# Kernel optimization log

Measured on AMD Instinct MI355X. Metric: run time of the kernel, lower is better.

## Reference

```python
import jax, jax.numpy as jnp
import numpy as np

N, E = 50000, 800000
IN, MAP, H, O = 256, 64, 4, 64
LEAKY_SLOPE = 0.2


def setup_inputs() -> dict:
    key = jax.random.key(0)
    ks = jax.random.split(key, 12)
    x = jax.random.normal(ks[0], (N, IN), dtype=jnp.float32)
    src = jax.random.randint(ks[1], (E,), 0, N, dtype=jnp.int32)
    dst = jax.random.randint(ks[2], (E,), 0, N, dtype=jnp.int32)
    s = 1.0 / np.sqrt(IN)
    W_gat = jax.random.normal(ks[3], (IN, H * O), dtype=jnp.float32) * s
    attn_l = jax.random.normal(ks[4], (H, O), dtype=jnp.float32) * 0.1
    attn_r = jax.random.normal(ks[5], (H, O), dtype=jnp.float32) * 0.1
    gate_m_W = jax.random.normal(ks[6], (IN, MAP), dtype=jnp.float32) * s
    gate_m_b = jnp.zeros((MAP,), dtype=jnp.float32)
    gate_fn_W = jax.random.normal(ks[7], (2 * IN + MAP, H), dtype=jnp.float32) * (1.0 / np.sqrt(2 * IN + MAP))
    gate_fn_b = jnp.zeros((H,), dtype=jnp.float32)
    merge_W = jax.random.normal(ks[8], (IN + O, O), dtype=jnp.float32) * (1.0 / np.sqrt(IN + O))
    merge_b = jnp.zeros((O,), dtype=jnp.float32)
    return {"x": x, "src": src, "dst": dst, "W_gat": W_gat, "attn_l": attn_l,
            "attn_r": attn_r, "gate_m_W": gate_m_W, "gate_m_b": gate_m_b,
            "gate_fn_W": gate_fn_W, "gate_fn_b": gate_fn_b,
            "merge_W": merge_W, "merge_b": merge_b}


def _forward(x, src, dst, W_gat, attn_l, attn_r, gate_m_W, gate_m_b,
             gate_fn_W, gate_fn_b, merge_W, merge_b):
    n = x.shape[0]
    # --- gate branch: gspmm mean of x, gspmm max of linear_z over in-neighbors ---
    deg = jax.ops.segment_sum(jnp.ones_like(dst, dtype=x.dtype), dst, num_segments=n)
    mean_z = jax.ops.segment_sum(x[src], dst, num_segments=n) / jnp.maximum(deg, 1.0)[:, None]
    z = x @ gate_m_W + gate_m_b  # [N, MAP]
    max_z = jax.ops.segment_max(z[src], dst, num_segments=n)
    max_z = jnp.where(deg[:, None] > 0, max_z, 0.0)  # empty neighborhoods -> 0
    nft = jnp.concatenate([x, max_z, mean_z], axis=1)  # [N, 2*IN+MAP]
    gate = jax.nn.sigmoid(nft @ gate_fn_W + gate_fn_b)  # [N, H]
    # --- GATConv ---
    feat = (x @ W_gat).reshape(n, H, O)  # [N, H, O]
    el = jnp.einsum('nho,ho->nh', feat, attn_l)
    er = jnp.einsum('nho,ho->nh', feat, attn_r)
    e = jax.nn.leaky_relu(el[src] + er[dst], negative_slope=LEAKY_SLOPE)  # [E, H]
    m = jax.ops.segment_max(e, dst, num_segments=n)  # [N, H]
    m = jnp.where(jnp.isfinite(m), m, 0.0)
    ex = jnp.exp(e - m[dst])  # [E, H]
    s = jax.ops.segment_sum(ex, dst, num_segments=n)  # [N, H]
    alpha = ex / jnp.maximum(s[dst], 1e-16)  # [E, H]
    attn_out = jax.ops.segment_sum(feat[src] * alpha[:, :, None], dst, num_segments=n)  # [N, H, O]
    # --- gated merge ---
    gated = (gate[:, :, None] * attn_out).mean(axis=1)  # [N, O]
    merge = jnp.concatenate([x, gated], axis=1) @ merge_W + merge_b  # [N, O]
    return merge


def reference(x, src, dst, W_gat, attn_l, attn_r, gate_m_W, gate_m_b,
              gate_fn_W, gate_fn_b, merge_W, merge_b):
    return _forward(x, src, dst, W_gat, attn_l, attn_r, gate_m_W, gate_m_b,
                    gate_fn_W, gate_fn_b, merge_W, merge_b)
```

## Files before the change

### kernel.cpp

```cpp
#include <hip/hip_runtime.h>
#include <math.h>

#define NN 50000
#define NE 800000
#define LEAKY 0.2f
#define NT 26
#define CAP 96
#define NBT (8 * NT * 64)
#define NB1 391
#define S1E 2048
#define NBUCK 196
#define EBMAX 5120
#define PREP_BLKS (55 + NB1)
#define GEMM_USED 1564
#define FUSE_BLKS 1764

typedef short bf16x8 __attribute__((ext_vector_type(8)));
typedef float f32x4 __attribute__((ext_vector_type(4)));
typedef float f32x2 __attribute__((ext_vector_type(2)));

__device__ __forceinline__ unsigned short f2bf(float f) {
  unsigned u = __float_as_uint(f);
  u += 0x7fffu + ((u >> 16) & 1u);
  return (unsigned short)(u >> 16);
}
__device__ __forceinline__ float leaky(float v) { return v > 0.0f ? v : LEAKY * v; }
__device__ __forceinline__ float rlf(float v, int l) {
  return __uint_as_float(__builtin_amdgcn_readlane(__float_as_uint(v), l));
}
__device__ __forceinline__ int rli(int v, int l) {
  return __builtin_amdgcn_readlane(v, l);
}

__device__ __forceinline__ bf16x8 cvt8(float4 fa, float4 fb) {
  unsigned r0, r1, r2, r3;
  asm("v_cvt_pk_bf16_f32 %0, %1, %2" : "=v"(r0) : "v"(fa.x), "v"(fa.y));
  asm("v_cvt_pk_bf16_f32 %0, %1, %2" : "=v"(r1) : "v"(fa.z), "v"(fa.w));
  asm("v_cvt_pk_bf16_f32 %0, %1, %2" : "=v"(r2) : "v"(fb.x), "v"(fb.y));
  asm("v_cvt_pk_bf16_f32 %0, %1, %2" : "=v"(r3) : "v"(fb.z), "v"(fb.w));
  union { uint4 u; bf16x8 v; } c;
  c.u = make_uint4(r0, r1, r2, r3);
  return c.v;
}

#if defined(__has_builtin)
#if __has_builtin(__builtin_amdgcn_cvt_pk_f32_fp8) && \
    __has_builtin(__builtin_amdgcn_cvt_pk_fp8_f32) && \
    __has_builtin(__builtin_amdgcn_cvt_f32_fp8)
#define FP8_HW 1
#endif
#endif

#ifdef FP8_HW
__device__ __forceinline__ unsigned char f2fp8(float v) {
  return (unsigned char)(__builtin_amdgcn_cvt_pk_fp8_f32(v, v, 0u, false) & 0xFF);
}
__device__ __forceinline__ f32x2 fp8x2_lo(unsigned int v) {
  return __builtin_amdgcn_cvt_pk_f32_fp8(v, false);
}
__device__ __forceinline__ f32x2 fp8x2_hi(unsigned int v) {
  return __builtin_amdgcn_cvt_pk_f32_fp8(v, true);
}
__device__ __forceinline__ float fp8one(unsigned int v) {
  return __builtin_amdgcn_cvt_f32_fp8(v, 0);
}
#else
__device__ __forceinline__ unsigned char f2fp8(float f) {
  unsigned u = __float_as_uint(f);
  unsigned s = (u >> 31) << 7;
  unsigned a = u & 0x7FFFFFFFu;
  if (a >= 0x43E00000u) return (unsigned char)(s | 0x7E);
  if (a < 0x3C800000u) {
    float m = __uint_as_float(a) * 512.0f;
    int q = (int)(m + 0.5f); if (q > 7) q = 7;
    return (unsigned char)(s | q);
  }
  a += 0x7FFFFu + ((a >> 20) & 1);
  unsigned e = ((a >> 23) & 0xFF) - 120;
  if (e > 15) return (unsigned char)(s | 0x7E);
  return (unsigned char)(s | (e << 3) | ((a >> 20) & 7));
}
__device__ __forceinline__ float fp8dec1(unsigned b) {
  unsigned s = (b & 0x80u) << 24;
  unsigned em = b & 0x7Fu;
  unsigned e4 = em >> 3, m3 = em & 7;
  float v = e4 ? __uint_as_float(((e4 + 120) << 23) | (m3 << 20))
               : (float)m3 * 0.001953125f;
  return __uint_as_float(__float_as_uint(v) ^ s);
}
__device__ __forceinline__ f32x2 fp8x2_lo(unsigned int v) {
  f32x2 r; r[0] = fp8dec1(v & 0xFF); r[1] = fp8dec1((v >> 8) & 0xFF); return r;
}
__device__ __forceinline__ f32x2 fp8x2_hi(unsigned int v) {
  f32x2 r; r[0] = fp8dec1((v >> 16) & 0xFF); r[1] = fp8dec1((v >> 24) & 0xFF); return r;
}
__device__ __forceinline__ float fp8one(unsigned int v) { return fp8dec1(v & 0xFF); }
#endif

__device__ __forceinline__ float dot64v(const float* __restrict__ w,
                                        const float* __restrict__ a) {
  float4 p0 = {0.f, 0.f, 0.f, 0.f};
#pragma unroll
  for (int o = 0; o < 64; o += 4) {
    float4 wv = *(const float4*)(w + o);
    float4 av = *(const float4*)(a + o);
    p0.x += wv.x * av.x; p0.y += wv.y * av.y;
    p0.z += wv.z * av.z; p0.w += wv.w * av.w;
  }
  return (p0.x + p0.y) + (p0.z + p0.w);
}
__device__ __forceinline__ float panel_w(int col, int k,
    const float* W_gat, const float* gate_m_W, const float* merge_W,
    const float* gate_fn_W, const float* attn_l, const float* attn_r) {
  if (col < 256)      return W_gat[k * 256 + (col & 3) * 64 + (col >> 2)];
  else if (col < 320) return gate_m_W[k * 64 + (col - 256)];
  else if (col < 384) return merge_W[k * 64 + (col - 320)];
  else if (col < 388) return gate_fn_W[k * 4 + (col - 384)];
  else if (col < 392) return gate_fn_W[(320 + k) * 4 + (col - 388)];
  else if (col < 396) {
    int h = col - 392;
    return dot64v(W_gat + k * 256 + h * 64, attn_l + h * 64);
  } else if (col < 400) {
    int h = col - 396;
    return dot64v(W_gat + k * 256 + h * 64, attn_r + h * 64);
  }
  return 0.0f;
}

__global__ __launch_bounds__(256) void k_prep_s1(
    const float* __restrict__ W_gat, const float* __restrict__ gate_m_W,
    const float* __restrict__ merge_W, const float* __restrict__ gate_fn_W,
    const float* __restrict__ attn_l, const float* __restrict__ attn_r,
    unsigned short* __restrict__ Btf, unsigned short* __restrict__ mWf,
    unsigned char* __restrict__ zq, float* __restrict__ epay,
    unsigned char* __restrict__ featq,
    const int* __restrict__ src, const int* __restrict__ dst,
    unsigned int* __restrict__ staged, unsigned short* __restrict__ bofs) {
  int b = blockIdx.x, tid = threadIdx.x;
  if (b < 54) {
    int idx = b * 256 + tid;
    if (idx < NBT) {
      int kq = idx / (NT * 64);
      int rem = idx - kq * (NT * 64);
      int t = rem >> 6, lane = rem & 63;
      int col = t * 16 + (lane & 15);
      int k = kq * 32 + (lane >> 4) * 8;
      unsigned short* o = Btf + (size_t)idx * 8;
#pragma unroll
      for (int i = 0; i < 8; ++i)
        o[i] = f2bf(panel_w(col, k + i, W_gat, gate_m_W, merge_W, gate_fn_W,
                            attn_l, attn_r));
    } else {
      int idx2 = idx - NBT;
      int kq = idx2 >> 8;
      int rem = idx2 & 255;
      int t = rem >> 6, lane = rem & 63;
      int col = t * 16 + (lane & 15);
      int k = kq * 32 + ((lane >> 4) & 3) * 8;
      unsigned short* o = mWf + (size_t)idx2 * 8;
#pragma unroll
      for (int i = 0; i < 8; ++i)
        o[i] = f2bf(merge_W[(size_t)(256 + k + i) * 64 + col]);
    }
  } else if (b == 54) {
    if (tid < 64) zq[(size_t)NN * 64 + tid] = 0xFE;
    if (tid < 8) epay[(size_t)NN * 8 + tid] = 0.0f;
    featq[(size_t)NN * 256 + tid] = 0;
  } else {
    __shared__ int hist[NBUCK], cntb[NBUCK], pfx[NBUCK], sc[256];
    __shared__ unsigned staged_l[S1E];
    int s1b = b - 55;
    int e0 = s1b * S1E;
    int cntE = NE - e0; if (cntE > S1E) cntE = S1E;
    for (int i = tid; i < NBUCK; i += 256) { hist[i] = 0; cntb[i] = 0; }
    __syncthreads();
    int myn[8], mys[8];
#pragma unroll
    for (int j = 0; j < 8; ++j) {
      int li = j * 256 + tid;
      bool valid = li < cntE;
      myn[j] = valid ? dst[e0 + li] : -1;
      mys[j] = valid ? src[e0 + li] : 0;
      if (valid) atomicAdd(&hist[myn[j] >> 8], 1);
    }
    __syncthreads();
    int v = (tid < NBUCK) ? hist[tid] : 0;
    sc[tid] = v; __syncthreads();
#pragma unroll
    for (int off = 1; off < 256; off <<= 1) {
      int t = (tid >= off) ? sc[tid - off] : 0;
      __syncthreads();
      sc[tid] += t;
      __syncthreads();
    }
    if (tid < NBUCK) pfx[tid] = sc[tid] - v;
    __syncthreads();
#pragma unroll
    for (int j = 0; j < 8; ++j) {
      if (myn[j] >= 0) {
        int bk = myn[j] >> 8;
        int p = pfx[bk] + atomicAdd(&cntb[bk], 1);
        staged_l[p] = ((unsigned)mys[j] << 8) | (unsigned)(myn[j] & 255);
      }
    }
    __syncthreads();
    for (int i = tid; i < cntE; i += 256) staged[(size_t)e0 + i] = staged_l[i];
    for (int i = tid; i < NBUCK + 1; i += 256)
      bofs[(size_t)s1b * (NBUCK + 1) + i] =
          (unsigned short)((i < NBUCK) ? pfx[i] : cntE);
  }
}

#define EBW 22528
union FusedLDS {
  unsigned short ldsB[2][13][64][8];
  struct {
    unsigned eb[EBMAX];
    int cnt2[256];
    int sc[256];
  } s2;
};

__global__ __launch_bounds__(256, 3) void k_gemm_s2(
    const float* __restrict__ x, const unsigned short* __restrict__ Btf,
    const float* __restrict__ gate_m_b,
    unsigned char* __restrict__ featq, unsigned char* __restrict__ zq,
    float* __restrict__ xm, float* __restrict__ gx, float* __restrict__ epay,
    float* __restrict__ erv,
    const unsigned int* __restrict__ staged, const unsigned short* __restrict__ bofs,
    int* __restrict__ deg, unsigned short* __restrict__ csr_src) {
  __shared__ FusedLDS L;
  int tid = threadIdx.x;
  int b = blockIdx.x;
  if (b % 9 == 8) {
    int bk = b / 9;
    int nb0 = bk << 8;
    int mycnt[2], myofs[2];
#pragma unroll
    for (int k = 0; k < 2; ++k) {
      int bi = tid + k * 256;
      if (bi < NB1) {
        int o  = bofs[(size_t)bi * (NBUCK + 1) + bk];
        int n1 = bofs[(size_t)bi * (NBUCK + 1) + bk + 1];
        myofs[k] = o; mycnt[k] = n1 - o;
      } else { myofs[k] = 0; mycnt[k] = 0; }
    }
    int lsum = mycnt[0] + mycnt[1];
    L.s2.sc[tid] = lsum; __syncthreads();
#pragma unroll
    for (int off = 1; off < 256; off <<= 1) {
      int t = (tid >= off) ? L.s2.sc[tid - off] : 0;
      __syncthreads();
      L.s2.sc[tid] += t;
      __syncthreads();
    }
    int base = L.s2.sc[tid] - lsum;
    int Eb = L.s2.sc[255];
    if (Eb > EBMAX) Eb = EBMAX;
    int pos = base;
#pragma unroll
    for (int k = 0; k < 2; ++k) {
      int bi = tid + k * 256;
      for (int c = 0; c < mycnt[k]; ++c) {
        if (pos < EBMAX)
          L.s2.eb[pos] = staged[(size_t)bi * S1E + myofs[k] + c];
        ++pos;
      }
    }
    __syncthreads();
    L.s2.cnt2[tid] = 0;
    __syncthreads();
    for (int i = tid; i < Eb; i += 256) {
      unsigned v = L.s2.eb[i];
      int nl = v & 255;
      int p = atomicAdd(&L.s2.cnt2[nl], 1);
      if (p < CAP)
        csr_src[(size_t)(nb0 + nl) * CAP + p] = (unsigned short)(v >> 8);
    }
    __syncthreads();
    int n = nb0 + tid;
    if (n < NN) {
      int d = L.s2.cnt2[tid];
      deg[n] = d < CAP ? d : CAP;
    }
    return;
  }
  int bq = b - b / 9;
  if (bq >= GEMM_USED) return;
  int rb = bq >> 1, ch = bq & 1;
  int lane = tid & 63, wave = tid >> 6;
  int m = lane & 15, kg = lane >> 4;
  int rowB = rb * 64;
  int t0 = ch * 13;
  int arow = rowB + wave * 16 + m;
  if (arow >= NN) arow = NN - 1;
  const float* aP = x + (size_t)arow * 256 + kg * 8;

  f32x4 acc[13];
  f32x4 zero = {0.f, 0.f, 0.f, 0.f};
#pragma unroll
  for (int t = 0; t < 13; ++t) acc[t] = zero;

  for (int t = wave; t < 13; t += 4)
    __builtin_amdgcn_global_load_lds(
        (const __attribute__((address_space(1))) unsigned int*)
            (Btf + ((size_t)(t0 + t)) * 512 + lane * 8),
        (__attribute__((address_space(3))) unsigned int*)(&L.ldsB[0][t][0][0]),
        16, 0, 0);
  float4 fa = *(const float4*)aP;
  float4 fb = *(const float4*)(aP + 4);
  __syncthreads();

#pragma unroll 1
  for (int kq = 0; kq < 8; ++kq) {
    int cur = kq & 1;
    int kqn = kq < 7 ? kq + 1 : 7;
    float4 fa_n = *(const float4*)(aP + kqn * 32);
    float4 fb_n = *(const float4*)(aP + kqn * 32 + 4);
    if (kq < 7) {
      for (int t = wave; t < 13; t += 4)
        __builtin_amdgcn_global_load_lds(
            (const __attribute__((address_space(1))) unsigned int*)
                (Btf + ((size_t)(kq + 1) * NT + t0 + t) * 512 + lane * 8),
            (__attribute__((address_space(3))) unsigned int*)
                (&L.ldsB[cur ^ 1][t][0][0]),
            16, 0, 0);
    }
    bf16x8 a = cvt8(fa, fb);
#pragma unroll
    for (int t = 0; t < 13; ++t) {
      bf16x8 bfr = *(const bf16x8*)&L.ldsB[cur][t][lane][0];
      acc[t] = __builtin_amdgcn_mfma_f32_16x16x32_bf16(a, bfr, acc[t], 0, 0, 0);
    }
    fa = fa_n; fb = fb_n;
    __syncthreads();
  }

  if (ch == 0) {
#pragma unroll
    for (int r = 0; r < 4; ++r) {
      int row = rowB + wave * 16 + kg * 4 + r;
      if (row >= NN) continue;
#pragma unroll
      for (int t = 0; t < 13; ++t)
        featq[(size_t)row * 256 + t * 16 + m] = f2fp8(acc[t][r]);
    }
  } else {
#pragma unroll
    for (int r = 0; r < 4; ++r) {
      int row = rowB + wave * 16 + kg * 4 + r;
      if (row >= NN) continue;
#pragma unroll
      for (int t = 0; t < 3; ++t)
        featq[(size_t)row * 256 + 208 + t * 16 + m] = f2fp8(acc[t][r]);
#pragma unroll
      for (int t = 3; t < 7; ++t) {
        int cc = (t - 3) * 16 + m;
        zq[(size_t)row * 64 + cc] = f2fp8(acc[t][r] + gate_m_b[cc]);
      }
#pragma unroll
      for (int t = 7; t < 11; ++t)
        xm[(size_t)row * 64 + (t - 7) * 16 + m] = acc[t][r];
      float v = acc[11][r];
      if (m < 4)       gx[(size_t)row * 4 + m] = v;
      else if (m < 8)  epay[(size_t)row * 8 + (m - 4) * 2 + 1] = v;
      else if (m < 12) epay[(size_t)row * 8 + (m - 8) * 2] = v;
      else             erv[(size_t)row * 4 + (m - 12)] = v;
    }
  }
}

__global__ __launch_bounds__(256) void k_node(
    const unsigned char* __restrict__ zq, const unsigned char* __restrict__ featq,
    const float* __restrict__ epay, const float* __restrict__ er,
    const float* __restrict__ gx,
    const int* __restrict__ deg, const unsigned short* __restrict__ csr_src,
    const float* __restrict__ gate_fn_W, const float* __restrict__ gate_fn_b,
    const unsigned short* __restrict__ mWf, const float* __restrict__ xm,
    const float* __restrict__ merge_b, float* __restrict__ out) {
  __shared__ float WzT[4][64];
  __shared__ float pbuf[4][16][4];
  __shared__ unsigned short gLDS[16][72];
  int tid = threadIdx.x;
  {
    int c = tid >> 2, h = tid & 3;
    WzT[h][c] = gate_fn_W[(256 + c) * 4 + h];
  }
  __syncthreads();

  int lane = tid & 63, wave = tid >> 6;
  int hh = lane >> 4, le = lane & 15;
  int rowbase = blockIdx.x * 16;
  int nodeBase = rowbase + wave * 4;
#pragma unroll 1
  for (int i = 0; i < 4; ++i) {
    int node = nodeBase + i;
    int dg = deg[node]; if (dg > CAP) dg = CAP;
    float gated = 0.0f;
    if (dg > 0) {
      int rs = node * CAP, re = rs + dg;
      float er_h = er[(size_t)node * 4 + hh];
      f32x2 A01 = {0.f, 0.f}, A23 = {0.f, 0.f};
      float psum = 0, usum = 0;
      float mz = -INFINITY;
      int jj = rs + le;
      int s_l = (jj < re) ? (int)csr_src[jj] : NN;
#pragma unroll 1
      for (int j0 = rs; j0 < re; j0 += 16) {
        int jn = j0 + 16 + le;
        int s_nx = (jn < re) ? (int)csr_src[jn] : NN;
        bool valid = (j0 + le) < re;
        float2 eu = *(const float2*)(epay + ((size_t)(unsigned)s_l << 3) + hh * 2);
        float p = valid ? __expf(leaky(eu.x + er_h)) : 0.0f;
        psum += p;
        usum += eu.y;
        pbuf[wave][le][hh] = p;
        unsigned int fvr[16];
        unsigned int zvr[16];
#pragma unroll
        for (int e2 = 0; e2 < 16; ++e2) {
          int s = rli(s_l, e2);
          fvr[e2] = *(const unsigned int*)(featq + ((size_t)(unsigned)s << 8) + lane * 4);
        }
#pragma unroll
        for (int e2 = 0; e2 < 16; ++e2) {
          int s = rli(s_l, e2);
          zvr[e2] = zq[((size_t)(unsigned)s << 6) + lane];
        }
#pragma unroll
        for (int e2 = 0; e2 < 16; ++e2) {
          float4 pv = *(const float4*)pbuf[wave][e2];
          f32x2 p01 = {pv.x, pv.y};
          f32x2 p23 = {pv.z, pv.w};
          A01 += p01 * fp8x2_lo(fvr[e2]);
          A23 += p23 * fp8x2_hi(fvr[e2]);
          mz = fmaxf(mz, fp8one(zvr[e2]));
        }
        s_l = s_nx;
      }
#pragma unroll
      for (int off = 1; off < 16; off <<= 1) {
        psum += __shfl_xor(psum, off, 64);
        usum += __shfl_xor(usum, off, 64);
      }
      float s0 = rlf(psum, 0),  s1 = rlf(psum, 16);
      float s2 = rlf(psum, 32), s3 = rlf(psum, 48);
      float su0 = rlf(usum, 0),  su1 = rlf(usum, 16);
      float su2 = rlf(usum, 32), su3 = rlf(usum, 48);

      float g[4];
#pragma unroll
      for (int h = 0; h < 4; ++h) {
        float t = mz * WzT[h][lane];
#pragma unroll
        for (int off = 32; off; off >>= 1) t += __shfl_xor(t, off, 64);
        g[h] = t;
      }
      float inv_deg = 1.0f / (float)dg;
      float4 gx4 = *(const float4*)(gx + (size_t)node * 4);
      float g0 = 1.0f / (1.0f + __expf(-(g[0] + gx4.x + su0 * inv_deg + gate_fn_b[0])));
      float g1 = 1.0f / (1.0f + __expf(-(g[1] + gx4.y + su1 * inv_deg + gate_fn_b[1])));
      float g2 = 1.0f / (1.0f + __expf(-(g[2] + gx4.z + su2 * inv_deg + gate_fn_b[2])));
      float g3 = 1.0f / (1.0f + __expf(-(g[3] + gx4.w + su3 * inv_deg + gate_fn_b[3])));
      gated = 0.25f * (g0 * A01[0] / s0 + g1 * A01[1] / s1 +
                       g2 * A23[0] / s2 + g3 * A23[1] / s3);
    }
    gLDS[wave * 4 + i][lane] = f2bf(gated);
  }
  __syncthreads();

  int m = lane & 15, kg = lane >> 4;
  f32x4 acc = {0.f, 0.f, 0.f, 0.f};
#pragma unroll
  for (int kq = 0; kq < 2; ++kq) {
    bf16x8 a = *(const bf16x8*)(&gLDS[m][kq * 32 + kg * 8]);
    bf16x8 b = *(const bf16x8*)(mWf + (((size_t)kq * 4 + wave) * 64 + lane) * 8);
    acc = __builtin_amdgcn_mfma_f32_16x16x32_bf16(a, b, acc, 0, 0, 0);
  }
  int c = wave * 16 + m;
  float mb = merge_b[c];
#pragma unroll
  for (int r = 0; r < 4; ++r) {
    int row = rowbase + kg * 4 + r;
    out[(size_t)row * 64 + c] = acc[r] + xm[(size_t)row * 64 + c] + mb;
  }
}

extern "C" void kernel_launch(void* const* d_in, const int* in_sizes, int n_in,
                              void* d_out, int out_size, void* d_ws, size_t ws_size,
                              hipStream_t stream) {
  const float* x         = (const float*)d_in[0];
  const int*   src       = (const int*)d_in[1];
  const int*   dst       = (const int*)d_in[2];
  const float* W_gat     = (const float*)d_in[3];
  const float* attn_l    = (const float*)d_in[4];
  const float* attn_r    = (const float*)d_in[5];
  const float* gate_m_W  = (const float*)d_in[6];
  const float* gate_m_b  = (const float*)d_in[7];
  const float* gate_fn_W = (const float*)d_in[8];
  const float* gate_fn_b = (const float*)d_in[9];
  const float* merge_W   = (const float*)d_in[10];
  const float* merge_b   = (const float*)d_in[11];
  float* out = (float*)d_out;

  char* ws = (char*)d_ws;
  size_t off = 0;
  auto alloc = [&](size_t bytes) -> void* {
    off = (off + 255) & ~(size_t)255;
    void* p = ws + off;
    off += bytes;
    return p;
  };
  int* deg       = (int*)alloc((size_t)NN * 4);
  unsigned short* csr_src = (unsigned short*)alloc((size_t)NN * CAP * 2);
  unsigned int* staged    = (unsigned int*)alloc((size_t)NE * 4);
  unsigned short* bofs    = (unsigned short*)alloc((size_t)NB1 * (NBUCK + 1) * 2);
  float* epay = (float*)alloc((size_t)(NN + 1) * 8 * 4);
  float* er   = (float*)alloc((size_t)NN * 4 * 4);
  float* gx   = (float*)alloc((size_t)NN * 4 * 4);
  float* xm   = (float*)alloc((size_t)NN * 64 * 4);
  unsigned char* zq    = (unsigned char*)alloc((size_t)(NN + 1) * 64);
  unsigned char* featq = (unsigned char*)alloc((size_t)(NN + 1) * 256);
  unsigned short* Btf    = (unsigned short*)alloc((size_t)NBT * 8 * 2);
  unsigned short* mWf    = (unsigned short*)alloc((size_t)512 * 8 * 2);

  k_prep_s1<<<PREP_BLKS, 256, 0, stream>>>(W_gat, gate_m_W, merge_W, gate_fn_W,
                                           attn_l, attn_r, Btf, mWf, zq, epay,
                                           featq, src, dst, staged, bofs);
  k_gemm_s2<<<FUSE_BLKS, 256, 0, stream>>>(x, Btf, gate_m_b,
                                           featq, zq, xm, gx, epay, er,
                                           staged, bofs, deg, csr_src);
  k_node<<<NN / 16, 256, 0, stream>>>(zq, featq, epay, er, gx, deg, csr_src,
                                      gate_fn_W, gate_fn_b, mWf, xm, merge_b, out);
}
```

Before: 234.2 us.

## Split GEMM into four column groups with register-resident B fragments instead of LDS

The fused GEMM kernel now splits each 64-row block's 26 output tiles into four column groups of 7 tiles (with overlap), rather than two halves of 13. B fragments are loaded straight from global memory into registers with double buffering, dropping the LDS staging and per-iteration barriers. The CSR-building blocks are moved to the first 196 block indices instead of being interleaved every ninth block. This gives more, lighter blocks with fewer accumulators to improve occupancy and remove sync stalls. The cost is redundant A-row loads across four blocks, some duplicated tile computation, and more global B traffic.

Result: no change. 238.5 us (+1.8%).

```diff
diff --git a/kernel.cpp b/kernel.cpp
--- a/kernel.cpp
+++ b/kernel.cpp
@@ -12,8 +12,8 @@
 #define NBUCK 196
 #define EBMAX 5120
 #define PREP_BLKS (55 + NB1)
-#define GEMM_USED 1564
-#define FUSE_BLKS 1764
+#define S2_BLKS 196
+#define FUSE_BLKS 3332
 
 typedef short bf16x8 __attribute__((ext_vector_type(8)));
 typedef float f32x4 __attribute__((ext_vector_type(4)));
@@ -211,16 +211,6 @@
   }
 }
 
-#define EBW 22528
-union FusedLDS {
-  unsigned short ldsB[2][13][64][8];
-  struct {
-    unsigned eb[EBMAX];
-    int cnt2[256];
-    int sc[256];
-  } s2;
-};
-
 __global__ __launch_bounds__(256, 3) void k_gemm_s2(
     const float* __restrict__ x, const unsigned short* __restrict__ Btf,
     const float* __restrict__ gate_m_b,
@@ -229,11 +219,15 @@
     float* __restrict__ erv,
     const unsigned int* __restrict__ staged, const unsigned short* __restrict__ bofs,
     int* __restrict__ deg, unsigned short* __restrict__ csr_src) {
-  __shared__ FusedLDS L;
+  __shared__ struct {
+    unsigned eb[EBMAX];
+    int cnt2[256];
+    int sc[256];
+  } L;
   int tid = threadIdx.x;
   int b = blockIdx.x;
-  if (b % 9 == 8) {
-    int bk = b / 9;
+  if (b < S2_BLKS) {
+    int bk = b;
     int nb0 = bk << 8;
     int mycnt[2], myofs[2];
 #pragma unroll
@@ -246,16 +240,16 @@
       } else { myofs[k] = 0; mycnt[k] = 0; }
     }
     int lsum = mycnt[0] + mycnt[1];
-    L.s2.sc[tid] = lsum; __syncthreads();
+    L.sc[tid] = lsum; __syncthreads();
 #pragma unroll
     for (int off = 1; off < 256; off <<= 1) {
-      int t = (tid >= off) ? L.s2.sc[tid - off] : 0;
+      int t = (tid >= off) ? L.sc[tid - off] : 0;
       __syncthreads();
-      L.s2.sc[tid] += t;
+      L.sc[tid] += t;
       __syncthreads();
     }
-    int base = L.s2.sc[tid] - lsum;
-    int Eb = L.s2.sc[255];
+    int base = L.sc[tid] - lsum;
+    int Eb = L.sc[255];
     if (Eb > EBMAX) Eb = EBMAX;
     int pos = base;
 #pragma unroll
@@ -263,109 +257,96 @@
       int bi = tid + k * 256;
       for (int c = 0; c < mycnt[k]; ++c) {
         if (pos < EBMAX)
-          L.s2.eb[pos] = staged[(size_t)bi * S1E + myofs[k] + c];
+          L.eb[pos] = staged[(size_t)bi * S1E + myofs[k] + c];
         ++pos;
       }
     }
     __syncthreads();
-    L.s2.cnt2[tid] = 0;
+    L.cnt2[tid] = 0;
     __syncthreads();
     for (int i = tid; i < Eb; i += 256) {
-      unsigned v = L.s2.eb[i];
+      unsigned v = L.eb[i];
       int nl = v & 255;
-      int p = atomicAdd(&L.s2.cnt2[nl], 1);
+      int p = atomicAdd(&L.cnt2[nl], 1);
       if (p < CAP)
         csr_src[(size_t)(nb0 + nl) * CAP + p] = (unsigned short)(v >> 8);
     }
     __syncthreads();
     int n = nb0 + tid;
     if (n < NN) {
-      int d = L.s2.cnt2[tid];
+      int d = L.cnt2[tid];
       deg[n] = d < CAP ? d : CAP;
     }
     return;
   }
-  int bq = b - b / 9;
-  if (bq >= GEMM_USED) return;
-  int rb = bq >> 1, ch = bq & 1;
+  int bq = b - S2_BLKS;
+  int rb = (bq >> 5) * 8 + (bq & 7);
+  if (rb >= 782) return;
+  int q = (bq >> 3) & 3;
+  int tstart = (q == 0) ? 0 : (q == 1) ? 7 : (q == 2) ? 13 : 19;
   int lane = tid & 63, wave = tid >> 6;
   int m = lane & 15, kg = lane >> 4;
   int rowB = rb * 64;
-  int t0 = ch * 13;
   int arow = rowB + wave * 16 + m;
   if (arow >= NN) arow = NN - 1;
   const float* aP = x + (size_t)arow * 256 + kg * 8;
-
-  f32x4 acc[13];
+  const unsigned short* bB = Btf + ((size_t)(tstart * 64 + lane)) * 8;
+
+  f32x4 acc[7];
   f32x4 zero = {0.f, 0.f, 0.f, 0.f};
 #pragma unroll
-  for (int t = 0; t < 13; ++t) acc[t] = zero;
-
-  for (int t = wave; t < 13; t += 4)
-    __builtin_amdgcn_global_load_lds(
-        (const __attribute__((address_space(1))) unsigned int*)
-            (Btf + ((size_t)(t0 + t)) * 512 + lane * 8),
-        (__attribute__((address_space(3))) unsigned int*)(&L.ldsB[0][t][0][0]),
-        16, 0, 0);
+  for (int t = 0; t < 7; ++t) acc[t] = zero;
+
+  bf16x8 bC[7], bN[7];
   float4 fa = *(const float4*)aP;
   float4 fb = *(const float4*)(aP + 4);
-  __syncthreads();
-
+#pragma unroll
+  for (int t = 0; t < 7; ++t)
+    bC[t] = *(const bf16x8*)(bB + (size_t)t * 512);
 #pragma unroll 1
-  for (int kq = 0; kq < 8; ++kq) {
-    int cur = kq & 1;
-    int kqn = kq < 7 ? kq + 1 : 7;
-    float4 fa_n = *(const float4*)(aP + kqn * 32);
-    float4 fb_n = *(const float4*)(aP + kqn * 32 + 4);
-    if (kq < 7) {
-      for (int t = wave; t < 13; t += 4)
-        __builtin_amdgcn_global_load_lds(
-            (const __attribute__((address_space(1))) unsigned int*)
-                (Btf + ((size_t)(kq + 1) * NT + t0 + t) * 512 + lane * 8),
-            (__attribute__((address_space(3))) unsigned int*)
-                (&L.ldsB[cur ^ 1][t][0][0]),
-            16, 0, 0);
-    }
-    bf16x8 a = cvt8(fa, fb);
-#pragma unroll
-    for (int t = 0; t < 13; ++t) {
-      bf16x8 bfr = *(const bf16x8*)&L.ldsB[cur][t][lane][0];
-      acc[t] = __builtin_amdgcn_mfma_f32_16x16x32_bf16(a, bfr, acc[t], 0, 0, 0);
-    }
-    fa = fa_n; fb = fb_n;
-    __syncthreads();
-  }
-
-  if (ch == 0) {
-#pragma unroll
-    for (int r = 0; r < 4; ++r) {
-      int row = rowB + wave * 16 + kg * 4 + r;
-      if (row >= NN) continue;
-#pragma unroll
-      for (int t = 0; t < 13; ++t)
-        featq[(size_t)row * 256 + t * 16 + m] = f2fp8(acc[t][r]);
-    }
-  } else {
-#pragma unroll
-    for (int r = 0; r < 4; ++r) {
-      int row = rowB + wave * 16 + kg * 4 + r;
-      if (row >= NN) continue;
-#pragma unroll
-      for (int t = 0; t < 3; ++t)
-        featq[(size_t)row * 256 + 208 + t * 16 + m] = f2fp8(acc[t][r]);
-#pragma unroll
-      for (int t = 3; t < 7; ++t) {
-        int cc = (t - 3) * 16 + m;
-        zq[(size_t)row * 64 + cc] = f2fp8(acc[t][r] + gate_m_b[cc]);
+  for (int kq = 0; kq < 8; kq += 2) {
+    float4 fa1 = *(const float4*)(aP + (kq + 1) * 32);
+    float4 fb1 = *(const float4*)(aP + (kq + 1) * 32 + 4);
+#pragma unroll
+    for (int t = 0; t < 7; ++t)
+      bN[t] = *(const bf16x8*)(bB + ((size_t)(kq + 1) * NT + t) * 512);
+    bf16x8 a0 = cvt8(fa, fb);
+#pragma unroll
+    for (int t = 0; t < 7; ++t)
+      acc[t] = __builtin_amdgcn_mfma_f32_16x16x32_bf16(a0, bC[t], acc[t], 0, 0, 0);
+    int kq2 = kq + 2 < 8 ? kq + 2 : 7;
+    fa = *(const float4*)(aP + kq2 * 32);
+    fb = *(const float4*)(aP + kq2 * 32 + 4);
+#pragma unroll
+    for (int t = 0; t < 7; ++t)
+      bC[t] = *(const bf16x8*)(bB + ((size_t)kq2 * NT + t) * 512);
+    bf16x8 a1 = cvt8(fa1, fb1);
+#pragma unroll
+    for (int t = 0; t < 7; ++t)
+      acc[t] = __builtin_amdgcn_mfma_f32_16x16x32_bf16(a1, bN[t], acc[t], 0, 0, 0);
+  }
+
+#pragma unroll
+  for (int r = 0; r < 4; ++r) {
+    int row = rowB + wave * 16 + kg * 4 + r;
+    if (row >= NN) continue;
+#pragma unroll
+    for (int t = 0; t < 7; ++t) {
+      int tg = tstart + t;
+      float v = acc[t][r];
+      if (tg < 16) {
+        featq[(size_t)row * 256 + tg * 16 + m] = f2fp8(v);
+      } else if (tg < 20) {
+        int cc = (tg - 16) * 16 + m;
+        zq[(size_t)row * 64 + cc] = f2fp8(v + gate_m_b[cc]);
+      } else if (tg < 24) {
+        xm[(size_t)row * 64 + (tg - 20) * 16 + m] = v;
+      } else if (tg == 24) {
+        if (m < 4)       gx[(size_t)row * 4 + m] = v;
+        else if (m < 8)  epay[(size_t)row * 8 + (m - 4) * 2 + 1] = v;
+        else if (m < 12) epay[(size_t)row * 8 + (m - 8) * 2] = v;
+        else             erv[(size_t)row * 4 + (m - 12)] = v;
       }
-#pragma unroll
-      for (int t = 7; t < 11; ++t)
-        xm[(size_t)row * 64 + (t - 7) * 16 + m] = acc[t][r];
-      float v = acc[11][r];
-      if (m < 4)       gx[(size_t)row * 4 + m] = v;
-      else if (m < 8)  epay[(size_t)row * 8 + (m - 4) * 2 + 1] = v;
-      else if (m < 12) epay[(size_t)row * 8 + (m - 8) * 2] = v;
-      else             erv[(size_t)row * 4 + (m - 12)] = v;
     }
   }
 }
```

## Fuse three phases into one persistent cooperative kernel with grid syncs

Applied to the files above, without the earlier changes.

Folds the prep/bucketing, GEMM/CSR-build and node-aggregation kernels into a single persistent cooperative kernel of 1024 blocks. The blocks loop over work items and separate the phases with grid.sync(), so two kernel launches and their gaps are gone. The shared memory for all phases is unified into one union, and there is a fallback to three separate kernels if a cooperative launch is unavailable. The risks are lower occupancy from the larger LDS union and launch_bounds of 4, grid-sync cost, and a fixed grid size that may not match the CU count. Interleaving CSR-build and GEMM blocks also changes from the old b%9 layout to CSR items first.

New measurement: 319.9 us. 1.37x slower.

```diff
diff --git a/kernel.cpp b/kernel.cpp
--- a/kernel.cpp
+++ b/kernel.cpp
@@ -1,5 +1,8 @@
 #include <hip/hip_runtime.h>
+#include <hip/hip_cooperative_groups.h>
 #include <math.h>
+
+namespace cg = cooperative_groups;
 
 #define NN 50000
 #define NE 800000
@@ -11,9 +14,11 @@
 #define S1E 2048
 #define NBUCK 196
 #define EBMAX 5120
-#define PREP_BLKS (55 + NB1)
+#define GRID_BLKS 1024
+#define PA_ITEMS (55 + NB1)
 #define GEMM_USED 1564
-#define FUSE_BLKS 1764
+#define PB_ITEMS (196 + GEMM_USED)
+#define PC_ITEMS 3125
 
 typedef short bf16x8 __attribute__((ext_vector_type(8)));
 typedef float f32x4 __attribute__((ext_vector_type(4)));
@@ -127,7 +132,21 @@
   return 0.0f;
 }
 
-__global__ __launch_bounds__(256) void k_prep_s1(
+union FusedLDS {
+  unsigned short ldsB[2][13][64][8];
+  struct {
+    int hist[NBUCK]; int cntb[NBUCK]; int pfx[NBUCK]; int sc[256];
+    unsigned staged_l[S1E];
+  } s1;
+  struct {
+    unsigned eb[EBMAX]; int cnt2[256]; int sc[256];
+  } s2;
+  struct {
+    float WzT[4][64]; float pbuf[4][16][4]; unsigned short gLDS[16][72];
+  } nd;
+};
+
+__device__ void phaseA_item(int it, int tid, FusedLDS& L,
     const float* __restrict__ W_gat, const float* __restrict__ gate_m_W,
     const float* __restrict__ merge_W, const float* __restrict__ gate_fn_W,
     const float* __restrict__ attn_l, const float* __restrict__ attn_r,
@@ -136,9 +155,8 @@
     unsigned char* __restrict__ featq,
     const int* __restrict__ src, const int* __restrict__ dst,
     unsigned int* __restrict__ staged, unsigned short* __restrict__ bofs) {
-  int b = blockIdx.x, tid = threadIdx.x;
-  if (b < 54) {
-    int idx = b * 256 + tid;
+  if (it < 54) {
+    int idx = it * 256 + tid;
     if (idx < NBT) {
       int kq = idx / (NT * 64);
       int rem = idx - kq * (NT * 64);
@@ -162,17 +180,15 @@
       for (int i = 0; i < 8; ++i)
         o[i] = f2bf(merge_W[(size_t)(256 + k + i) * 64 + col]);
     }
-  } else if (b == 54) {
+  } else if (it == 54) {
     if (tid < 64) zq[(size_t)NN * 64 + tid] = 0xFE;
     if (tid < 8) epay[(size_t)NN * 8 + tid] = 0.0f;
     featq[(size_t)NN * 256 + tid] = 0;
   } else {
-    __shared__ int hist[NBUCK], cntb[NBUCK], pfx[NBUCK], sc[256];
-    __shared__ unsigned staged_l[S1E];
-    int s1b = b - 55;
+    int s1b = it - 55;
     int e0 = s1b * S1E;
     int cntE = NE - e0; if (cntE > S1E) cntE = S1E;
-    for (int i = tid; i < NBUCK; i += 256) { hist[i] = 0; cntb[i] = 0; }
+    for (int i = tid; i < NBUCK; i += 256) { L.s1.hist[i] = 0; L.s1.cntb[i] = 0; }
     __syncthreads();
     int myn[8], mys[8];
 #pragma unroll
@@ -181,47 +197,38 @@
       bool valid = li < cntE;
       myn[j] = valid ? dst[e0 + li] : -1;
       mys[j] = valid ? src[e0 + li] : 0;
-      if (valid) atomicAdd(&hist[myn[j] >> 8], 1);
-    }
-    __syncthreads();
-    int v = (tid < NBUCK) ? hist[tid] : 0;
-    sc[tid] = v; __syncthreads();
+      if (valid) atomicAdd(&L.s1.hist[myn[j] >> 8], 1);
+    }
+    __syncthreads();
+    int v = (tid < NBUCK) ? L.s1.hist[tid] : 0;
+    L.s1.sc[tid] = v; __syncthreads();
 #pragma unroll
     for (int off = 1; off < 256; off <<= 1) {
-      int t = (tid >= off) ? sc[tid - off] : 0;
+      int t = (tid >= off) ? L.s1.sc[tid - off] : 0;
       __syncthreads();
-      sc[tid] += t;
+      L.s1.sc[tid] += t;
       __syncthreads();
     }
-    if (tid < NBUCK) pfx[tid] = sc[tid] - v;
+    if (tid < NBUCK) L.s1.pfx[tid] = L.s1.sc[tid] - v;
     __syncthreads();
 #pragma unroll
     for (int j = 0; j < 8; ++j) {
       if (myn[j] >= 0) {
         int bk = myn[j] >> 8;
-        int p = pfx[bk] + atomicAdd(&cntb[bk], 1);
-        staged_l[p] = ((unsigned)mys[j] << 8) | (unsigned)(myn[j] & 255);
+        int p = L.s1.pfx[bk] + atomicAdd(&L.s1.cntb[bk], 1);
+        L.s1.staged_l[p] = ((unsigned)mys[j] << 8) | (unsigned)(myn[j] & 255);
       }
     }
     __syncthreads();
-    for (int i = tid; i < cntE; i += 256) staged[(size_t)e0 + i] = staged_l[i];
+    for (int i = tid; i < cntE; i += 256) staged[(size_t)e0 + i] = L.s1.staged_l[i];
     for (int i = tid; i < NBUCK + 1; i += 256)
       bofs[(size_t)s1b * (NBUCK + 1) + i] =
-          (unsigned short)((i < NBUCK) ? pfx[i] : cntE);
-  }
-}
-
-#define EBW 22528
-union FusedLDS {
-  unsigned short ldsB[2][13][64][8];
-  struct {
-    unsigned eb[EBMAX];
-    int cnt2[256];
-    int sc[256];
-  } s2;
-};
-
-__global__ __launch_bounds__(256, 3) void k_gemm_s2(
+          (unsigned short)((i < NBUCK) ? L.s1.pfx[i] : cntE);
+    __syncthreads();
+  }
+}
+
+__device__ void phaseB_item(int it, int tid, FusedLDS& L,
     const float* __restrict__ x, const unsigned short* __restrict__ Btf,
     const float* __restrict__ gate_m_b,
     unsigned char* __restrict__ featq, unsigned char* __restrict__ zq,
@@ -229,11 +236,8 @@
     float* __restrict__ erv,
     const unsigned int* __restrict__ staged, const unsigned short* __restrict__ bofs,
     int* __restrict__ deg, unsigned short* __restrict__ csr_src) {
-  __shared__ FusedLDS L;
-  int tid = threadIdx.x;
-  int b = blockIdx.x;
-  if (b % 9 == 8) {
-    int bk = b / 9;
+  if (it < 196) {
+    int bk = it;
     int nb0 = bk << 8;
     int mycnt[2], myofs[2];
 #pragma unroll
@@ -283,10 +287,10 @@
       int d = L.s2.cnt2[tid];
       deg[n] = d < CAP ? d : CAP;
     }
+    __syncthreads();
     return;
   }
-  int bq = b - b / 9;
-  if (bq >= GEMM_USED) return;
+  int bq = it - 196;
   int rb = bq >> 1, ch = bq & 1;
   int lane = tid & 63, wave = tid >> 6;
   int m = lane & 15, kg = lane >> 4;
@@ -370,7 +374,7 @@
   }
 }
 
-__global__ __launch_bounds__(256) void k_node(
+__device__ void phaseC_block(int nb, int tid, FusedLDS& L,
     const unsigned char* __restrict__ zq, const unsigned char* __restrict__ featq,
     const float* __restrict__ epay, const float* __restrict__ er,
     const float* __restrict__ gx,
@@ -378,19 +382,15 @@
     const float* __restrict__ gate_fn_W, const float* __restrict__ gate_fn_b,
     const unsigned short* __restrict__ mWf, const float* __restrict__ xm,
     const float* __restrict__ merge_b, float* __restrict__ out) {
-  __shared__ float WzT[4][64];
-  __shared__ float pbuf[4][16][4];
-  __shared__ unsigned short gLDS[16][72];
-  int tid = threadIdx.x;
   {
     int c = tid >> 2, h = tid & 3;
-    WzT[h][c] = gate_fn_W[(256 + c) * 4 + h];
+    L.nd.WzT[h][c] = gate_fn_W[(256 + c) * 4 + h];
   }
   __syncthreads();
 
   int lane = tid & 63, wave = tid >> 6;
   int hh = lane >> 4, le = lane & 15;
-  int rowbase = blockIdx.x * 16;
+  int rowbase = nb * 16;
   int nodeBase = rowbase + wave * 4;
 #pragma unroll 1
   for (int i = 0; i < 4; ++i) {
@@ -414,7 +414,7 @@
         float p = valid ? __expf(leaky(eu.x + er_h)) : 0.0f;
         psum += p;
         usum += eu.y;
-        pbuf[wave][le][hh] = p;
+        L.nd.pbuf[wave][le][hh] = p;
         unsigned int fvr[16];
         unsigned int zvr[16];
 #pragma unroll
@@ -429,7 +429,7 @@
         }
 #pragma unroll
         for (int e2 = 0; e2 < 16; ++e2) {
-          float4 pv = *(const float4*)pbuf[wave][e2];
+          float4 pv = *(const float4*)L.nd.pbuf[wave][e2];
           f32x2 p01 = {pv.x, pv.y};
           f32x2 p23 = {pv.z, pv.w};
           A01 += p01 * fp8x2_lo(fvr[e2]);
@@ -451,7 +451,7 @@
       float g[4];
 #pragma unroll
       for (int h = 0; h < 4; ++h) {
-        float t = mz * WzT[h][lane];
+        float t = mz * L.nd.WzT[h][lane];
 #pragma unroll
         for (int off = 32; off; off >>= 1) t += __shfl_xor(t, off, 64);
         g[h] = t;
@@ -465,7 +465,7 @@
       gated = 0.25f * (g0 * A01[0] / s0 + g1 * A01[1] / s1 +
                        g2 * A23[0] / s2 + g3 * A23[1] / s3);
     }
-    gLDS[wave * 4 + i][lane] = f2bf(gated);
+    L.nd.gLDS[wave * 4 + i][lane] = f2bf(gated);
   }
   __syncthreads();
 
@@ -473,7 +473,7 @@
   f32x4 acc = {0.f, 0.f, 0.f, 0.f};
 #pragma unroll
   for (int kq = 0; kq < 2; ++kq) {
-    bf16x8 a = *(const bf16x8*)(&gLDS[m][kq * 32 + kg * 8]);
+    bf16x8 a = *(const bf16x8*)(&L.nd.gLDS[m][kq * 32 + kg * 8]);
     bf16x8 b = *(const bf16x8*)(mWf + (((size_t)kq * 4 + wave) * 64 + lane) * 8);
     acc = __builtin_amdgcn_mfma_f32_16x16x32_bf16(a, b, acc, 0, 0, 0);
   }
@@ -484,6 +484,64 @@
     int row = rowbase + kg * 4 + r;
     out[(size_t)row * 64 + c] = acc[r] + xm[(size_t)row * 64 + c] + mb;
   }
+  __syncthreads();
+}
+
+__global__ __launch_bounds__(256, 4) void k_fused(
+    const float* x, const int* src, const int* dst,
+    const float* W_gat, const float* attn_l, const float* attn_r,
+    const float* gate_m_W, const float* gate_m_b,
+    const float* gate_fn_W, const float* gate_fn_b,
+    const float* merge_W, const float* merge_b, float* out,
+    unsigned short* Btf, unsigned short* mWf,
+    unsigned char* zq, unsigned char* featq, float* epay, float* erv,
+    float* gx, float* xm,
+    unsigned* staged, unsigned short* bofs,
+    int* deg, unsigned short* csr_src) {
+  cg::grid_group grid = cg::this_grid();
+  __shared__ FusedLDS L;
+  int tid = threadIdx.x;
+  for (int it = blockIdx.x; it < PA_ITEMS; it += GRID_BLKS)
+    phaseA_item(it, tid, L, W_gat, gate_m_W, merge_W, gate_fn_W, attn_l, attn_r,
+                Btf, mWf, zq, epay, featq, src, dst, staged, bofs);
+  grid.sync();
+  for (int it = blockIdx.x; it < PB_ITEMS; it += GRID_BLKS)
+    phaseB_item(it, tid, L, x, Btf, gate_m_b, featq, zq, xm, gx, epay, erv,
+                staged, bofs, deg, csr_src);
+  grid.sync();
+  for (int it = blockIdx.x; it < PC_ITEMS; it += GRID_BLKS)
+    phaseC_block(it, tid, L, zq, featq, epay, erv, gx, deg, csr_src,
+                 gate_fn_W, gate_fn_b, mWf, xm, merge_b, out);
+}
+
+__global__ __launch_bounds__(256, 4) void k_pA(
+    const float* W_gat, const float* gate_m_W, const float* merge_W,
+    const float* gate_fn_W, const float* attn_l, const float* attn_r,
+    unsigned short* Btf, unsigned short* mWf, unsigned char* zq, float* epay,
+    unsigned char* featq, const int* src, const int* dst,
+    unsigned* staged, unsigned short* bofs) {
+  __shared__ FusedLDS L;
+  phaseA_item(blockIdx.x, threadIdx.x, L, W_gat, gate_m_W, merge_W, gate_fn_W,
+              attn_l, attn_r, Btf, mWf, zq, epay, featq, src, dst, staged, bofs);
+}
+__global__ __launch_bounds__(256, 4) void k_pB(
+    const float* x, const unsigned short* Btf, const float* gate_m_b,
+    unsigned char* featq, unsigned char* zq, float* xm, float* gx, float* epay,
+    float* erv, const unsigned* staged, const unsigned short* bofs,
+    int* deg, unsigned short* csr_src) {
+  __shared__ FusedLDS L;
+  phaseB_item(blockIdx.x, threadIdx.x, L, x, Btf, gate_m_b, featq, zq, xm, gx,
+              epay, erv, staged, bofs, deg, csr_src);
+}
+__global__ __launch_bounds__(256, 4) void k_pC(
+    const unsigned char* zq, const unsigned char* featq, const float* epay,
+    const float* er, const float* gx, const int* deg,
+    const unsigned short* csr_src, const float* gate_fn_W,
+    const float* gate_fn_b, const unsigned short* mWf, const float* xm,
+    const float* merge_b, float* out) {
+  __shared__ FusedLDS L;
+  phaseC_block(blockIdx.x, threadIdx.x, L, zq, featq, epay, er, gx, deg, csr_src,
+               gate_fn_W, gate_fn_b, mWf, xm, merge_b, out);
 }
 
 extern "C" void kernel_launch(void* const* d_in, const int* in_sizes, int n_in,
@@ -524,12 +582,33 @@
   unsigned short* Btf    = (unsigned short*)alloc((size_t)NBT * 8 * 2);
   unsigned short* mWf    = (unsigned short*)alloc((size_t)512 * 8 * 2);
 
-  k_prep_s1<<<PREP_BLKS, 256, 0, stream>>>(W_gat, gate_m_W, merge_W, gate_fn_W,
-                                           attn_l, attn_r, Btf, mWf, zq, epay,
-                                           featq, src, dst, staged, bofs);
-  k_gemm_s2<<<FUSE_BLKS, 256, 0, stream>>>(x, Btf, gate_m_b,
-                                           featq, zq, xm, gx, epay, er,
-                                           staged, bofs, deg, csr_src);
-  k_node<<<NN / 16, 256, 0, stream>>>(zq, featq, epay, er, gx, deg, csr_src,
-                                      gate_fn_W, gate_fn_b, mWf, xm, merge_b, out);
-}
+  static int coop = -1;
+  if (coop < 0) {
+    int v = 0;
+    hipDeviceGetAttribute(&v, hipDeviceAttributeCooperativeLaunch, 0);
+    coop = v;
+  }
+
+  if (coop) {
+    void* args[] = {
+      (void*)&x, (void*)&src, (void*)&dst, (void*)&W_gat, (void*)&attn_l,
+      (void*)&attn_r, (void*)&gate_m_W, (void*)&gate_m_b, (void*)&gate_fn_W,
+      (void*)&gate_fn_b, (void*)&merge_W, (void*)&merge_b, (void*)&out,
+      (void*)&Btf, (void*)&mWf, (void*)&zq, (void*)&featq, (void*)&epay,
+      (void*)&er, (void*)&gx, (void*)&xm, (void*)&staged, (void*)&bofs,
+      (void*)&deg, (void*)&csr_src };
+    hipError_t rc = hipLaunchCooperativeKernel((const void*)k_fused,
+                                               dim3(GRID_BLKS), dim3(256),
+                                               args, 0, stream);
+    if (rc == hipSuccess) return;
+    coop = 0;
+  }
+
+  k_pA<<<PA_ITEMS, 256, 0, stream>>>(W_gat, gate_m_W, merge_W, gate_fn_W,
+                                     attn_l, attn_r, Btf, mWf, zq, epay,
+                                     featq, src, dst, staged, bofs);
+  k_pB<<<PB_ITEMS, 256, 0, stream>>>(x, Btf, gate_m_b, featq, zq, xm, gx,
+                                     epay, er, staged, bofs, deg, csr_src);
+  k_pC<<<PC_ITEMS, 256, 0, stream>>>(zq, featq, epay, er, gx, deg, csr_src,
+                                     gate_fn_W, gate_fn_b, mWf, xm, merge_b, out);
+}
```
